# Kernel tuning notes

Measured on AMD Instinct MI355X. Metric: run time of the kernel, lower is better.

The kernel has to match this reference:

```python
import jax, jax.numpy as jnp
import numpy as np

EPS = 1e-12  # torch F.normalize clamp

N, C, H, W = 32, 128, 128, 128
K = 64  # num_clusters


def setup_inputs() -> dict:
    key = jax.random.key(0)
    k1, k2, k3 = jax.random.split(key, 3)
    x = jax.random.normal(k1, (N, C, H, W), dtype=jnp.float32)
    conv_w = jax.random.normal(k2, (K, C), dtype=jnp.float32) * 0.1  # 1x1 conv weight, no bias
    centroids = jax.random.uniform(k3, (K, C), dtype=jnp.float32)   # torch.rand init
    return {"x": x, "conv_w": conv_w, "centroids": centroids}


def reference(x, conv_w, centroids):
    n, c = x.shape[:2]
    xf = x.reshape(n, c, -1)                       # [N, C, S], S = H*W
    # 1x1 conv == per-location matmul over channels
    soft_assign = jnp.einsum('kc,ncs->nks', conv_w, xf)
    soft_assign = jax.nn.softmax(soft_assign, axis=1)   # softmax over clusters
    # vlad[n,k,c] = sum_s a[n,k,s] * (x[n,c,s] - centroid[k,c])
    #            = (a @ x^T) - (sum_s a) * centroid   (avoids per-cluster residual tensors)
    vlad = jnp.einsum('nks,ncs->nkc', soft_assign, xf) \
           - soft_assign.sum(axis=-1)[..., None] * centroids[None, :, :]
    # intra-normalization over descriptor dim
    vlad = vlad / jnp.maximum(jnp.linalg.norm(vlad, axis=2, keepdims=True), EPS)
    flat = vlad.reshape(n, -1)                     # [N, K*C]
    flat = flat / jnp.maximum(jnp.linalg.norm(flat, axis=1, keepdims=True), EPS)
    return flat
```

## Files before the change

kernel.cpp:

```cpp
#include <hip/hip_runtime.h>

#define N_ 32
#define C_ 128
#define K_ 64
#define S_ 16384
#define TS 64
#define NBPN 24
#define NTILES (S_/TS)
#define NBLK (N_*NBPN)
#define XS 136
#define WS 136
#define PS 72
#define EPS 1e-12f

typedef __attribute__((ext_vector_type(8))) _Float16 half8;
typedef __attribute__((ext_vector_type(4))) _Float16 half4;
typedef __attribute__((ext_vector_type(4))) float floatx4;

__device__ __forceinline__ int swz(int row, int c) {
  return (((c >> 4) ^ (row & 7)) << 4) | (c & 15);
}

#define BAR_LDS()                                            \
  do {                                                       \
    __builtin_amdgcn_sched_barrier(0);                       \
    asm volatile("s_waitcnt lgkmcnt(0)" ::: "memory");       \
    __builtin_amdgcn_s_barrier();                            \
    __builtin_amdgcn_sched_barrier(0);                       \
  } while (0)

template <bool SLAB>
__global__ __launch_bounds__(256, 4) void vlad_main(
    const float* __restrict__ x, const float* __restrict__ w,
    float* __restrict__ vlad_out, float* __restrict__ asum_out) {
  __shared__ _Float16 sXT[TS * XS];
  __shared__ _Float16 sW[K_ * WS];
  __shared__ _Float16 sP[K_ * PS];
  __shared__ float sRed[4 * K_];

  const int tid = threadIdx.x;
  const int lane = tid & 63;
  const int wv = tid >> 6;
  const int lm = lane & 15;
  const int quad = lane >> 4;

  const int bid = blockIdx.x;
  const int n = bid / NBPN;
  const int j = bid % NBPN;
  const int ts = (j * NTILES) / NBPN;
  const int te = ((j + 1) * NTILES) / NBPN;

  for (int idx = tid; idx < K_ * C_; idx += 256) {
    int kc = idx >> 7, c = idx & 127;
    sW[kc * WS + swz(kc, c)] = (_Float16)w[idx];
  }

  floatx4 acc[2][4];
#pragma unroll
  for (int i = 0; i < 2; ++i)
#pragma unroll
    for (int k = 0; k < 4; ++k) acc[i][k] = (floatx4){0.f, 0.f, 0.f, 0.f};
  float accA[4] = {0.f, 0.f, 0.f, 0.f};

  const float* xn = x + (size_t)n * C_ * S_;
  const float* xrow[2];
  xrow[0] = xn + (size_t)((2 * wv + 0) * 16 + lm) * S_;
  xrow[1] = xn + (size_t)((2 * wv + 1) * 16 + lm) * S_;

  float4 gx[2][2][2];
#pragma unroll
  for (int ci = 0; ci < 2; ++ci)
#pragma unroll
    for (int sl = 0; sl < 2; ++sl) {
      const float* p = xrow[ci] + ts * TS + sl * 32 + quad * 8;
      gx[ci][sl][0] = *(const float4*)p;
      gx[ci][sl][1] = *(const float4*)(p + 4);
    }

  __syncthreads();

  for (int t = ts; t < te; ++t) {
    half8 hx[2][2];
#pragma unroll
    for (int ci = 0; ci < 2; ++ci)
#pragma unroll
      for (int sl = 0; sl < 2; ++sl) {
        half8 h;
        h[0] = (_Float16)gx[ci][sl][0].x; h[1] = (_Float16)gx[ci][sl][0].y;
        h[2] = (_Float16)gx[ci][sl][0].z; h[3] = (_Float16)gx[ci][sl][0].w;
        h[4] = (_Float16)gx[ci][sl][1].x; h[5] = (_Float16)gx[ci][sl][1].y;
        h[6] = (_Float16)gx[ci][sl][1].z; h[7] = (_Float16)gx[ci][sl][1].w;
        hx[ci][sl] = h;
      }
#pragma unroll
    for (int ci = 0; ci < 2; ++ci) {
#pragma unroll
      for (int sl = 0; sl < 2; ++sl) {
        const int key = sl * 4 + quad;
        const int blk = (2 * wv + ci) ^ key;
        const int base = (sl * 32 + quad * 8) * XS + blk * 16 + lm;
#pragma unroll
        for (int jj = 0; jj < 8; ++jj)
          sXT[base + jj * XS] = hx[ci][sl][jj];
      }
    }

    if (t + 1 < te) {
#pragma unroll
      for (int ci = 0; ci < 2; ++ci)
#pragma unroll
        for (int sl = 0; sl < 2; ++sl) {
          const float* p = xrow[ci] + (t + 1) * TS + sl * 32 + quad * 8;
          gx[ci][sl][0] = *(const float4*)p;
          gx[ci][sl][1] = *(const float4*)(p + 4);
        }
    }
    BAR_LDS();

    floatx4 D[4];
#pragma unroll
    for (int k = 0; k < 4; ++k) D[k] = (floatx4){0.f, 0.f, 0.f, 0.f};
    const int srow = wv * 16 + lm;
    const int rkey = (srow >> 3) & 7;
#pragma unroll
    for (int ks = 0; ks < 4; ++ks) {
      const int cb = ks * 32 + quad * 8;
      const int blk = (cb >> 4) ^ rkey;
      half8 Af = *(const half8*)&sXT[srow * XS + blk * 16 + (cb & 15)];
#pragma unroll
      for (int kt = 0; kt < 4; ++kt) {
        const int krow = kt * 16 + lm;
        half8 Wf = *(const half8*)&sW[krow * WS + swz(krow, ks * 32 + quad * 8)];
        D[kt] = __builtin_amdgcn_mfma_f32_16x16x32_f16(Af, Wf, D[kt], 0, 0, 0);
      }
    }

#pragma unroll
    for (int r = 0; r < 4; ++r) {
      float e0 = __expf(D[0][r]), e1 = __expf(D[1][r]),
            e2 = __expf(D[2][r]), e3 = __expf(D[3][r]);
      float sum = e0 + e1 + e2 + e3;
      sum += __shfl_xor(sum, 1);
      sum += __shfl_xor(sum, 2);
      sum += __shfl_xor(sum, 4);
      sum += __shfl_xor(sum, 8);
      float inv = 1.f / sum;
      D[0][r] = e0 * inv; D[1][r] = e1 * inv;
      D[2][r] = e2 * inv; D[3][r] = e3 * inv;
    }
#pragma unroll
    for (int kt = 0; kt < 4; ++kt) {
      accA[kt] += D[kt][0] + D[kt][1] + D[kt][2] + D[kt][3];
      half4 hp = {(_Float16)D[kt][0], (_Float16)D[kt][1],
                  (_Float16)D[kt][2], (_Float16)D[kt][3]};
      *(half4*)&sP[(kt * 16 + lm) * PS + wv * 16 + quad * 4] = hp;
    }
    BAR_LDS();

#pragma unroll
    for (int sl = 0; sl < 2; ++sl) {
      half8 Pf[4];
#pragma unroll
      for (int kt = 0; kt < 4; ++kt)
        Pf[kt] = *(const half8*)&sP[(kt * 16 + lm) * PS + sl * 32 + quad * 8];
#pragma unroll
      for (int ci = 0; ci < 2; ++ci)
#pragma unroll
        for (int kt = 0; kt < 4; ++kt)
          acc[ci][kt] = __builtin_amdgcn_mfma_f32_16x16x32_f16(
              Pf[kt], hx[ci][sl], acc[ci][kt], 0, 0, 0);
    }
  }

  float* vb = vlad_out + (SLAB ? (size_t)bid : (size_t)n) * (K_ * C_);
#pragma unroll
  for (int ci = 0; ci < 2; ++ci) {
    const int c = (2 * wv + ci) * 16 + lm;
#pragma unroll
    for (int kt = 0; kt < 4; ++kt) {
      const int kc0 = kt * 16 + quad * 4;
#pragma unroll
      for (int r = 0; r < 4; ++r) {
        if (SLAB) {
          vb[(size_t)(kc0 + r) * C_ + c] = acc[ci][kt][r];
        } else {
          atomicAdd(vb + (size_t)(kc0 + r) * C_ + c, acc[ci][kt][r]);
        }
      }
    }
  }

#pragma unroll
  for (int kt = 0; kt < 4; ++kt) {
    float v = accA[kt];
    v += __shfl_xor(v, 16);
    v += __shfl_xor(v, 32);
    if (quad == 0) sRed[wv * K_ + kt * 16 + lm] = v;
  }
  __syncthreads();
  if (tid < K_) {
    float s = sRed[tid] + sRed[K_ + tid] + sRed[2 * K_ + tid] + sRed[3 * K_ + tid];
    if (SLAB) asum_out[(size_t)bid * K_ + tid] = s;
    else atomicAdd(asum_out + n * K_ + tid, s);
  }
}

template <bool SLAB>
__global__ __launch_bounds__(128) void vlad_intra(
    const float* __restrict__ vlad_in, const float* __restrict__ asum_in,
    const float* __restrict__ cent, float* __restrict__ vlad_norm,
    float* __restrict__ gnorm) {
  const int bid = blockIdx.x;
  const int n = bid >> 6, k = bid & 63;
  const int c = threadIdx.x;

  float v, a;
  if (SLAB) {
    v = 0.f; a = 0.f;
#pragma unroll 4
    for (int ch = 0; ch < NBPN; ++ch) {
      v += vlad_in[((size_t)(n * NBPN + ch) * K_ + k) * C_ + c];
      a += asum_in[(n * NBPN + ch) * K_ + k];
    }
  } else {
    v = vlad_in[((size_t)(n * K_ + k)) * C_ + c];
    a = asum_in[n * K_ + k];
  }
  v -= a * cent[k * C_ + c];

  float ss = v * v;
  ss += __shfl_xor(ss, 1);  ss += __shfl_xor(ss, 2);  ss += __shfl_xor(ss, 4);
  ss += __shfl_xor(ss, 8);  ss += __shfl_xor(ss, 16); ss += __shfl_xor(ss, 32);
  __shared__ float red[2];
  if ((threadIdx.x & 63) == 0) red[threadIdx.x >> 6] = ss;
  __syncthreads();
  float total = red[0] + red[1];
  float nrm = fmaxf(sqrtf(total), EPS);
  vlad_norm[((size_t)(n * K_ + k)) * C_ + c] = v / nrm;
  if (threadIdx.x == 0) atomicAdd(gnorm + n, total / (nrm * nrm));
}

__global__ __launch_bounds__(256) void vlad_final(
    const float* __restrict__ vlad_norm, const float* __restrict__ gnorm,
    float* __restrict__ out) {
  const int idx = blockIdx.x * 256 + threadIdx.x;
  if (idx >= N_ * K_ * C_) return;
  float g = gnorm[idx >> 13];
  out[idx] = vlad_norm[idx] / fmaxf(sqrtf(g), EPS);
}

extern "C" void kernel_launch(void* const* d_in, const int* in_sizes, int n_in,
                              void* d_out, int out_size, void* d_ws, size_t ws_size,
                              hipStream_t stream) {
  const float* x    = (const float*)d_in[0];
  const float* w    = (const float*)d_in[1];
  const float* cent = (const float*)d_in[2];
  float* out = (float*)d_out;

  const size_t slab_f = (size_t)NBLK * K_ * C_;
  const size_t asum_f = (size_t)NBLK * K_;
  const size_t norm_f = (size_t)N_ * K_ * C_;
  const size_t need = (slab_f + asum_f + norm_f + N_) * sizeof(float);

  if (ws_size >= need) {
    float* slab  = (float*)d_ws;
    float* asums = slab + slab_f;
    float* vnorm = asums + asum_f;
    float* gnorm = vnorm + norm_f;
    hipMemsetAsync(gnorm, 0, N_ * sizeof(float), stream);
    vlad_main<true><<<dim3(NBLK), dim3(256), 0, stream>>>(x, w, slab, asums);
    vlad_intra<true><<<dim3(N_ * K_), dim3(128), 0, stream>>>(slab, asums, cent, vnorm, gnorm);
    vlad_final<<<dim3((N_ * K_ * C_ + 255) / 256), dim3(256), 0, stream>>>(vnorm, gnorm, out);
  } else {
    float* vlad_acc = (float*)d_ws;
    float* asum_g   = vlad_acc + norm_f;
    float* gnorm    = asum_g + N_ * K_;
    hipMemsetAsync(d_ws, 0, (norm_f + N_ * K_ + N_) * sizeof(float), stream);
    vlad_main<false><<<dim3(NBLK), dim3(256), 0, stream>>>(x, w, vlad_acc, asum_g);
    vlad_intra<false><<<dim3(N_ * K_), dim3(128), 0, stream>>>(vlad_acc, asum_g, cent, vlad_acc, gnorm);
    vlad_final<<<dim3((N_ * K_ * C_ + 255) / 256), dim3(256), 0, stream>>>(vlad_acc, gnorm, out);
  }
}
```

Before: 398.0 us.

## Replace LDS row padding with XOR swizzles and use 32 blocks per sample

Removes the padded strides of the shared-memory tiles (XS/WS 136→128, PS 72→64) and instead XOR-swizzles the X-transpose, weight and softmax-probability tiles to avoid bank conflicts. It also aliases the reduction scratch onto the X tile and changes the split to 32 blocks per sample, each with an equal number of tiles. This shrinks LDS per block, which may allow more blocks per CU, and removes uneven tile splits. The risk is that the new swizzles may still conflict or break correctness if the write and read mappings do not match, and reusing sXT for sRed requires proper barriers.

Result: slower. 485.0 us (+21.8%).

```diff
diff --git a/kernel.cpp b/kernel.cpp
--- a/kernel.cpp
+++ b/kernel.cpp
@@ -5,12 +5,13 @@
 #define K_ 64
 #define S_ 16384
 #define TS 64
-#define NBPN 24
+#define NBPN 32
 #define NTILES (S_/TS)
+#define TPB (NTILES/NBPN)
 #define NBLK (N_*NBPN)
-#define XS 136
-#define WS 136
-#define PS 72
+#define XS 128
+#define WS 128
+#define PS 64
 #define EPS 1e-12f
 
 typedef __attribute__((ext_vector_type(8))) _Float16 half8;
@@ -36,7 +37,7 @@
   __shared__ _Float16 sXT[TS * XS];
   __shared__ _Float16 sW[K_ * WS];
   __shared__ _Float16 sP[K_ * PS];
-  __shared__ float sRed[4 * K_];
+  float* sRed = (float*)sXT;
 
   const int tid = threadIdx.x;
   const int lane = tid & 63;
@@ -45,10 +46,10 @@
   const int quad = lane >> 4;
 
   const int bid = blockIdx.x;
-  const int n = bid / NBPN;
-  const int j = bid % NBPN;
-  const int ts = (j * NTILES) / NBPN;
-  const int te = ((j + 1) * NTILES) / NBPN;
+  const int n = bid >> 5;
+  const int j = bid & 31;
+  const int ts = j * TPB;
+  const int te = ts + TPB;
 
   for (int idx = tid; idx < K_ * C_; idx += 256) {
     int kc = idx >> 7, c = idx & 127;
@@ -97,11 +98,11 @@
 #pragma unroll
       for (int sl = 0; sl < 2; ++sl) {
         const int key = sl * 4 + quad;
-        const int blk = (2 * wv + ci) ^ key;
-        const int base = (sl * 32 + quad * 8) * XS + blk * 16 + lm;
+        const int cblk = 2 * wv + ci;
+        const int base = (sl * 32 + quad * 8) * XS + lm;
 #pragma unroll
         for (int jj = 0; jj < 8; ++jj)
-          sXT[base + jj * XS] = hx[ci][sl][jj];
+          sXT[base + jj * XS + (((cblk ^ key ^ jj)) << 4)] = hx[ci][sl][jj];
       }
     }
 
@@ -121,12 +122,11 @@
 #pragma unroll
     for (int k = 0; k < 4; ++k) D[k] = (floatx4){0.f, 0.f, 0.f, 0.f};
     const int srow = wv * 16 + lm;
-    const int rkey = (srow >> 3) & 7;
+    const int rk = ((srow >> 3) & 7) ^ (srow & 7);
 #pragma unroll
     for (int ks = 0; ks < 4; ++ks) {
-      const int cb = ks * 32 + quad * 8;
-      const int blk = (cb >> 4) ^ rkey;
-      half8 Af = *(const half8*)&sXT[srow * XS + blk * 16 + (cb & 15)];
+      const int blk = (ks * 2 + (quad >> 1)) ^ rk;
+      half8 Af = *(const half8*)&sXT[srow * XS + blk * 16 + (quad & 1) * 8];
 #pragma unroll
       for (int kt = 0; kt < 4; ++kt) {
         const int krow = kt * 16 + lm;
@@ -153,7 +153,8 @@
       accA[kt] += D[kt][0] + D[kt][1] + D[kt][2] + D[kt][3];
       half4 hp = {(_Float16)D[kt][0], (_Float16)D[kt][1],
                   (_Float16)D[kt][2], (_Float16)D[kt][3]};
-      *(half4*)&sP[(kt * 16 + lm) * PS + wv * 16 + quad * 4] = hp;
+      const int pg = (wv * 2 + (quad >> 1)) ^ (lm & 7);
+      *(half4*)&sP[(kt * 16 + lm) * PS + pg * 8 + (quad & 1) * 4] = hp;
     }
     BAR_LDS();
 
@@ -161,8 +162,10 @@
     for (int sl = 0; sl < 2; ++sl) {
       half8 Pf[4];
 #pragma unroll
-      for (int kt = 0; kt < 4; ++kt)
-        Pf[kt] = *(const half8*)&sP[(kt * 16 + lm) * PS + sl * 32 + quad * 8];
+      for (int kt = 0; kt < 4; ++kt) {
+        const int pg = (sl * 4 + quad) ^ (lm & 7);
+        Pf[kt] = *(const half8*)&sP[(kt * 16 + lm) * PS + pg * 8];
+      }
 #pragma unroll
       for (int ci = 0; ci < 2; ++ci)
 #pragma unroll
```

## Remove LDS staging of x and probabilities; redundant per-wave logits with DPP shuffles

Applied to the files above, without the earlier changes.

Rewrites the main kernel so each wave loads x directly from global memory in the register layouts both MFMA stages need. The shared-memory transpose buffer, the probability buffer and the two per-tile barriers go away. Every wave now recomputes all 64 logits for its 32 positions and redistributes the softmax probabilities through lane shuffles, with DPP row reductions for the softmax sum. The grid is 16 blocks per image with 2 blocks per CU, and a padding array limits occupancy. The cost is duplicated projection MFMA work and strided, uncoalesced global loads for the transposed x operand.

After: 437.5 us. 1.1x slower.

```diff
diff --git a/kernel.cpp b/kernel.cpp
--- a/kernel.cpp
+++ b/kernel.cpp
@@ -4,204 +4,210 @@
 #define C_ 128
 #define K_ 64
 #define S_ 16384
-#define TS 64
-#define NBPN 24
-#define NTILES (S_/TS)
-#define NBLK (N_*NBPN)
-#define XS 136
-#define WS 136
-#define PS 72
+#define NBPB 16
+#define NBLK (N_*NBPB)
+#define SPB 32
+#define WS 128
 #define EPS 1e-12f
 
 typedef __attribute__((ext_vector_type(8))) _Float16 half8;
-typedef __attribute__((ext_vector_type(4))) _Float16 half4;
+typedef __attribute__((ext_vector_type(2))) _Float16 half2v;
 typedef __attribute__((ext_vector_type(4))) float floatx4;
+typedef __attribute__((ext_vector_type(4))) int intx4;
 
 __device__ __forceinline__ int swz(int row, int c) {
   return (((c >> 4) ^ (row & 7)) << 4) | (c & 15);
 }
 
-#define BAR_LDS()                                            \
-  do {                                                       \
-    __builtin_amdgcn_sched_barrier(0);                       \
-    asm volatile("s_waitcnt lgkmcnt(0)" ::: "memory");       \
-    __builtin_amdgcn_s_barrier();                            \
-    __builtin_amdgcn_sched_barrier(0);                       \
-  } while (0)
+__device__ __forceinline__ float rowsum16(float v) {
+  int b;
+  b = __builtin_amdgcn_mov_dpp(__builtin_bit_cast(int, v), 0x128, 0xF, 0xF, true);
+  v += __builtin_bit_cast(float, b);
+  b = __builtin_amdgcn_mov_dpp(__builtin_bit_cast(int, v), 0x124, 0xF, 0xF, true);
+  v += __builtin_bit_cast(float, b);
+  b = __builtin_amdgcn_mov_dpp(__builtin_bit_cast(int, v), 0x122, 0xF, 0xF, true);
+  v += __builtin_bit_cast(float, b);
+  b = __builtin_amdgcn_mov_dpp(__builtin_bit_cast(int, v), 0x121, 0xF, 0xF, true);
+  v += __builtin_bit_cast(float, b);
+  return v;
+}
 
 template <bool SLAB>
-__global__ __launch_bounds__(256, 4) void vlad_main(
+__global__ __launch_bounds__(256, 2) void vlad_main(
     const float* __restrict__ x, const float* __restrict__ w,
     float* __restrict__ vlad_out, float* __restrict__ asum_out) {
-  __shared__ _Float16 sXT[TS * XS];
   __shared__ _Float16 sW[K_ * WS];
-  __shared__ _Float16 sP[K_ * PS];
-  __shared__ float sRed[4 * K_];
+  __shared__ float sPad[9472];
 
   const int tid = threadIdx.x;
   const int lane = tid & 63;
   const int wv = tid >> 6;
   const int lm = lane & 15;
-  const int quad = lane >> 4;
+  const int q = lane >> 4;
 
   const int bid = blockIdx.x;
-  const int n = bid / NBPN;
-  const int j = bid % NBPN;
-  const int ts = (j * NTILES) / NBPN;
-  const int te = ((j + 1) * NTILES) / NBPN;
+  const int n = bid >> 4;
+  const int bj = bid & 15;
 
   for (int idx = tid; idx < K_ * C_; idx += 256) {
     int kc = idx >> 7, c = idx & 127;
     sW[kc * WS + swz(kc, c)] = (_Float16)w[idx];
   }
+  if (w[0] > 1e30f) sPad[tid] = w[0];
+  __syncthreads();
 
   floatx4 acc[2][4];
 #pragma unroll
-  for (int i = 0; i < 2; ++i)
-#pragma unroll
-    for (int k = 0; k < 4; ++k) acc[i][k] = (floatx4){0.f, 0.f, 0.f, 0.f};
+  for (int ci = 0; ci < 2; ++ci)
+#pragma unroll
+    for (int kt = 0; kt < 4; ++kt) acc[ci][kt] = (floatx4){0.f, 0.f, 0.f, 0.f};
   float accA[4] = {0.f, 0.f, 0.f, 0.f};
 
   const float* xn = x + (size_t)n * C_ * S_;
-  const float* xrow[2];
-  xrow[0] = xn + (size_t)((2 * wv + 0) * 16 + lm) * S_;
-  xrow[1] = xn + (size_t)((2 * wv + 1) * 16 + lm) * S_;
-
-  float4 gx[2][2][2];
-#pragma unroll
-  for (int ci = 0; ci < 2; ++ci)
-#pragma unroll
-    for (int sl = 0; sl < 2; ++sl) {
-      const float* p = xrow[ci] + ts * TS + sl * 32 + quad * 8;
-      gx[ci][sl][0] = *(const float4*)p;
-      gx[ci][sl][1] = *(const float4*)(p + 4);
-    }
-
-  __syncthreads();
-
-  for (int t = ts; t < te; ++t) {
-    half8 hx[2][2];
-#pragma unroll
-    for (int ci = 0; ci < 2; ++ci)
-#pragma unroll
-      for (int sl = 0; sl < 2; ++sl) {
-        half8 h;
-        h[0] = (_Float16)gx[ci][sl][0].x; h[1] = (_Float16)gx[ci][sl][0].y;
-        h[2] = (_Float16)gx[ci][sl][0].z; h[3] = (_Float16)gx[ci][sl][0].w;
-        h[4] = (_Float16)gx[ci][sl][1].x; h[5] = (_Float16)gx[ci][sl][1].y;
-        h[6] = (_Float16)gx[ci][sl][1].z; h[7] = (_Float16)gx[ci][sl][1].w;
-        hx[ci][sl] = h;
-      }
+  const float* pA = xn + (size_t)(q * 8) * S_ + lm;
+  const float* pB = xn + (size_t)(wv * 32 + lm) * S_ + q * 8;
+
+  for (int i = 0; i < SPB; ++i) {
+    const int s0 = (bj * SPB + i) * 32;
+    const float* pAs = pA + s0;
+
+    float xa[2][2][8];
+#pragma unroll
+    for (int ks = 0; ks < 2; ++ks)
+#pragma unroll
+      for (int sg = 0; sg < 2; ++sg)
+#pragma unroll
+        for (int j = 0; j < 8; ++j)
+          xa[ks][sg][j] = pAs[(size_t)(ks * 32 + j) * S_ + sg * 16];
+
+    float4 xb[2][2];
 #pragma unroll
     for (int ci = 0; ci < 2; ++ci) {
-#pragma unroll
-      for (int sl = 0; sl < 2; ++sl) {
-        const int key = sl * 4 + quad;
-        const int blk = (2 * wv + ci) ^ key;
-        const int base = (sl * 32 + quad * 8) * XS + blk * 16 + lm;
-#pragma unroll
-        for (int jj = 0; jj < 8; ++jj)
-          sXT[base + jj * XS] = hx[ci][sl][jj];
-      }
-    }
-
-    if (t + 1 < te) {
-#pragma unroll
-      for (int ci = 0; ci < 2; ++ci)
-#pragma unroll
-        for (int sl = 0; sl < 2; ++sl) {
-          const float* p = xrow[ci] + (t + 1) * TS + sl * 32 + quad * 8;
-          gx[ci][sl][0] = *(const float4*)p;
-          gx[ci][sl][1] = *(const float4*)(p + 4);
-        }
-    }
-    BAR_LDS();
-
-    floatx4 D[4];
-#pragma unroll
-    for (int k = 0; k < 4; ++k) D[k] = (floatx4){0.f, 0.f, 0.f, 0.f};
-    const int srow = wv * 16 + lm;
-    const int rkey = (srow >> 3) & 7;
+      const float* p = pB + (size_t)(ci * 16) * S_ + s0;
+      xb[ci][0] = *(const float4*)p;
+      xb[ci][1] = *(const float4*)(p + 4);
+    }
+
+    floatx4 D[2][4];
+#pragma unroll
+    for (int sg = 0; sg < 2; ++sg)
+#pragma unroll
+      for (int kt = 0; kt < 4; ++kt) D[sg][kt] = (floatx4){0.f, 0.f, 0.f, 0.f};
+
 #pragma unroll
     for (int ks = 0; ks < 4; ++ks) {
-      const int cb = ks * 32 + quad * 8;
-      const int blk = (cb >> 4) ^ rkey;
-      half8 Af = *(const half8*)&sXT[srow * XS + blk * 16 + (cb & 15)];
+      half8 Wf[4];
 #pragma unroll
       for (int kt = 0; kt < 4; ++kt) {
         const int krow = kt * 16 + lm;
-        half8 Wf = *(const half8*)&sW[krow * WS + swz(krow, ks * 32 + quad * 8)];
-        D[kt] = __builtin_amdgcn_mfma_f32_16x16x32_f16(Af, Wf, D[kt], 0, 0, 0);
-      }
-    }
-
-#pragma unroll
-    for (int r = 0; r < 4; ++r) {
-      float e0 = __expf(D[0][r]), e1 = __expf(D[1][r]),
-            e2 = __expf(D[2][r]), e3 = __expf(D[3][r]);
-      float sum = e0 + e1 + e2 + e3;
-      sum += __shfl_xor(sum, 1);
-      sum += __shfl_xor(sum, 2);
-      sum += __shfl_xor(sum, 4);
-      sum += __shfl_xor(sum, 8);
-      float inv = 1.f / sum;
-      D[0][r] = e0 * inv; D[1][r] = e1 * inv;
-      D[2][r] = e2 * inv; D[3][r] = e3 * inv;
-    }
+        Wf[kt] = *(const half8*)&sW[krow * WS + swz(krow, ks * 32 + q * 8)];
+      }
+      half8 Af[2];
+#pragma unroll
+      for (int sg = 0; sg < 2; ++sg)
+#pragma unroll
+        for (int j = 0; j < 8; ++j)
+          Af[sg][j] = (_Float16)xa[ks & 1][sg][j];
+      if (ks < 2) {
+#pragma unroll
+        for (int sg = 0; sg < 2; ++sg)
+#pragma unroll
+          for (int j = 0; j < 8; ++j)
+            xa[ks & 1][sg][j] = pAs[(size_t)((ks + 2) * 32 + j) * S_ + sg * 16];
+      }
+#pragma unroll
+      for (int sg = 0; sg < 2; ++sg)
+#pragma unroll
+        for (int kt = 0; kt < 4; ++kt)
+          D[sg][kt] = __builtin_amdgcn_mfma_f32_16x16x32_f16(Af[sg], Wf[kt], D[sg][kt], 0, 0, 0);
+    }
+
+#pragma unroll
+    for (int sg = 0; sg < 2; ++sg)
+#pragma unroll
+      for (int r = 0; r < 4; ++r) {
+        float e0 = __expf(D[sg][0][r]), e1 = __expf(D[sg][1][r]),
+              e2 = __expf(D[sg][2][r]), e3 = __expf(D[sg][3][r]);
+        float inv = 1.f / rowsum16(e0 + e1 + e2 + e3);
+        D[sg][0][r] = e0 * inv; D[sg][1][r] = e1 * inv;
+        D[sg][2][r] = e2 * inv; D[sg][3][r] = e3 * inv;
+      }
+    if (wv == 0) {
+#pragma unroll
+      for (int kt = 0; kt < 4; ++kt)
+        accA[kt] += D[0][kt][0] + D[0][kt][1] + D[0][kt][2] + D[0][kt][3]
+                  + D[1][kt][0] + D[1][kt][1] + D[1][kt][2] + D[1][kt][3];
+    }
+
+    half8 xbh[2];
+#pragma unroll
+    for (int ci = 0; ci < 2; ++ci) {
+      xbh[ci][0] = (_Float16)xb[ci][0].x; xbh[ci][1] = (_Float16)xb[ci][0].y;
+      xbh[ci][2] = (_Float16)xb[ci][0].z; xbh[ci][3] = (_Float16)xb[ci][0].w;
+      xbh[ci][4] = (_Float16)xb[ci][1].x; xbh[ci][5] = (_Float16)xb[ci][1].y;
+      xbh[ci][6] = (_Float16)xb[ci][1].z; xbh[ci][7] = (_Float16)xb[ci][1].w;
+    }
+
+    half8 Pb[4];
+    const int srcBase = ((lane >> 4) & 1) * 32 + lm;
 #pragma unroll
     for (int kt = 0; kt < 4; ++kt) {
-      accA[kt] += D[kt][0] + D[kt][1] + D[kt][2] + D[kt][3];
-      half4 hp = {(_Float16)D[kt][0], (_Float16)D[kt][1],
-                  (_Float16)D[kt][2], (_Float16)D[kt][3]};
-      *(half4*)&sP[(kt * 16 + lm) * PS + wv * 16 + quad * 4] = hp;
-    }
-    BAR_LDS();
-
-#pragma unroll
-    for (int sl = 0; sl < 2; ++sl) {
-      half8 Pf[4];
-#pragma unroll
-      for (int kt = 0; kt < 4; ++kt)
-        Pf[kt] = *(const half8*)&sP[(kt * 16 + lm) * PS + sl * 32 + quad * 8];
-#pragma unroll
-      for (int ci = 0; ci < 2; ++ci)
-#pragma unroll
-        for (int kt = 0; kt < 4; ++kt)
-          acc[ci][kt] = __builtin_amdgcn_mfma_f32_16x16x32_f16(
-              Pf[kt], hx[ci][sl], acc[ci][kt], 0, 0, 0);
-    }
-  }
-
-  float* vb = vlad_out + (SLAB ? (size_t)bid : (size_t)n) * (K_ * C_);
-#pragma unroll
-  for (int ci = 0; ci < 2; ++ci) {
-    const int c = (2 * wv + ci) * 16 + lm;
+      int u0[2], u1[2];
+#pragma unroll
+      for (int rp = 0; rp < 2; ++rp) {
+        half2v h0 = {(_Float16)D[0][kt][2 * rp], (_Float16)D[0][kt][2 * rp + 1]};
+        half2v h1 = {(_Float16)D[1][kt][2 * rp], (_Float16)D[1][kt][2 * rp + 1]};
+        u0[rp] = __builtin_bit_cast(int, h0);
+        u1[rp] = __builtin_bit_cast(int, h1);
+      }
+      int wd[4];
+#pragma unroll
+      for (int rr = 0; rr < 4; ++rr) {
+        const int src = srcBase + (rr >> 1) * 16;
+        const int a0 = __shfl(u0[rr & 1], src);
+        const int a1 = __shfl(u1[rr & 1], src);
+        wd[rr] = (lane < 32) ? a0 : a1;
+      }
+      intx4 wq = {wd[0], wd[1], wd[2], wd[3]};
+      Pb[kt] = __builtin_bit_cast(half8, wq);
+    }
+
+#pragma unroll
+    for (int ci = 0; ci < 2; ++ci)
+#pragma unroll
+      for (int kt = 0; kt < 4; ++kt)
+        acc[ci][kt] = __builtin_amdgcn_mfma_f32_16x16x32_f16(xbh[ci], Pb[kt], acc[ci][kt], 0, 0, 0);
+  }
+
+  if (SLAB) {
+    float* vb = vlad_out + (size_t)bid * (K_ * C_);
+#pragma unroll
+    for (int ci = 0; ci < 2; ++ci)
+#pragma unroll
+      for (int kt = 0; kt < 4; ++kt)
+        *(floatx4*)&vb[(size_t)(kt * 16 + lm) * C_ + wv * 32 + ci * 16 + q * 4] = acc[ci][kt];
+  } else {
+    float* vb = vlad_out + (size_t)n * (K_ * C_);
+#pragma unroll
+    for (int ci = 0; ci < 2; ++ci)
+#pragma unroll
+      for (int kt = 0; kt < 4; ++kt)
+#pragma unroll
+        for (int r = 0; r < 4; ++r)
+          atomicAdd(vb + (size_t)(kt * 16 + lm) * C_ + wv * 32 + ci * 16 + q * 4 + r,
+                    acc[ci][kt][r]);
+  }
+  if (wv == 0) {
 #pragma unroll
     for (int kt = 0; kt < 4; ++kt) {
-      const int kc0 = kt * 16 + quad * 4;
-#pragma unroll
-      for (int r = 0; r < 4; ++r) {
-        if (SLAB) {
-          vb[(size_t)(kc0 + r) * C_ + c] = acc[ci][kt][r];
-        } else {
-          atomicAdd(vb + (size_t)(kc0 + r) * C_ + c, acc[ci][kt][r]);
-        }
-      }
-    }
-  }
-
-#pragma unroll
-  for (int kt = 0; kt < 4; ++kt) {
-    float v = accA[kt];
-    v += __shfl_xor(v, 16);
-    v += __shfl_xor(v, 32);
-    if (quad == 0) sRed[wv * K_ + kt * 16 + lm] = v;
-  }
-  __syncthreads();
-  if (tid < K_) {
-    float s = sRed[tid] + sRed[K_ + tid] + sRed[2 * K_ + tid] + sRed[3 * K_ + tid];
-    if (SLAB) asum_out[(size_t)bid * K_ + tid] = s;
-    else atomicAdd(asum_out + n * K_ + tid, s);
+      float v = accA[kt];
+      v += __shfl_xor(v, 16);
+      v += __shfl_xor(v, 32);
+      if (lane < 16) {
+        if (SLAB) asum_out[bid * K_ + kt * 16 + lane] = v;
+        else atomicAdd(asum_out + n * K_ + kt * 16 + lane, v);
+      }
+    }
   }
 }
 
@@ -218,9 +224,9 @@
   if (SLAB) {
     v = 0.f; a = 0.f;
 #pragma unroll 4
-    for (int ch = 0; ch < NBPN; ++ch) {
-      v += vlad_in[((size_t)(n * NBPN + ch) * K_ + k) * C_ + c];
-      a += asum_in[(n * NBPN + ch) * K_ + k];
+    for (int ch = 0; ch < NBPB; ++ch) {
+      v += vlad_in[((size_t)(n * NBPB + ch) * K_ + k) * C_ + c];
+      a += asum_in[(n * NBPB + ch) * K_ + k];
     }
   } else {
     v = vlad_in[((size_t)(n * K_ + k)) * C_ + c];
```
